# Optimization experiments

Hardware: AMD Instinct MI355X
Metric: run time of the kernel (lower is better)

## Reference

```python
import jax, jax.numpy as jnp
import numpy as np

N_BINS = 10
P = 2


def setup_inputs() -> dict:
    key = jax.random.key(0)
    k1, k2 = jax.random.split(key)
    N, C = 1_000_000, 80
    probas = jax.random.uniform(k1, (N, C), dtype=jnp.float32)
    labels = jax.random.randint(k2, (N,), 0, C, dtype=jnp.int64 if jax.config.jax_enable_x64 else jnp.int32)
    return {"probas": probas, "labels": labels}


def reference(probas, labels):
    n, c = probas.shape
    bins = jnp.linspace(0.0, 1.0, N_BINS + 1)
    # torch loop uses half-open-at-left bins: bin_start < p <= bin_end.
    # searchsorted(side='left') finds first bin edge >= p; subtract 1 -> bin index.
    # p == 0 maps to -1 (belongs to no bin), matching the torch masks.
    bin_idx = jnp.searchsorted(bins, probas, side="left") - 1  # [N, C]
    # route out-of-range (p==0) samples to a per-class trash slot N_BINS
    slots = N_BINS + 1
    seg = jnp.where(bin_idx >= 0, bin_idx, N_BINS) + jnp.arange(c)[None, :] * slots  # [N, C]
    flat_seg = seg.reshape(-1)
    num_seg = c * slots

    ones = jnp.ones((n * c,), dtype=jnp.float32)
    counts = jax.ops.segment_sum(ones, flat_seg, num_segments=num_seg).reshape(c, slots)[:, :N_BINS]
    sum_p = jax.ops.segment_sum(probas.reshape(-1), flat_seg, num_segments=num_seg).reshape(c, slots)[:, :N_BINS]
    correct = (labels[:, None] == jnp.arange(c)[None, :]).astype(jnp.float32)  # [N, C]
    sum_acc = jax.ops.segment_sum(correct.reshape(-1), flat_seg, num_segments=num_seg).reshape(c, slots)[:, :N_BINS]

    nonempty = counts > 0  # [C, N_BINS]
    denom = jnp.maximum(counts, 1.0)
    confs = sum_p / denom   # mean confidence per (class, bin); NaN slots masked below
    accs = sum_acc / denom  # accuracy per (class, bin)

    # calibration_error with bin_weight='samples': probas_bin = n_samples / nansum(n_samples)
    probas_bin = counts / jnp.sum(counts, axis=1, keepdims=True)
    # sq_ce per class = nansum(probas_bin * (conf - acc)**P)  (empty bins contribute 0)
    sq_ce = jnp.sum(jnp.where(nonempty, probas_bin * (confs - accs) ** P, 0.0), axis=1)  # [C]
    mce = jnp.mean(sq_ce) ** (1.0 / P)
    return mce
```

## Files before the change

kernel.cpp:

```cpp
#include <hip/hip_runtime.h>

#define NBINS  10
#define NCLS   80
#define NSLOTS (NCLS * NBINS)
#define QS     262144.0f

__global__ void __launch_bounds__(256)
mce_accum(const float4* __restrict__ probas,
          const int*    __restrict__ labels,
          unsigned long long* __restrict__ g_pack,
          unsigned int nvec) {
    __shared__ unsigned long long s_pack[NSLOTS];
    for (int i = threadIdx.x; i < NSLOTS; i += 256) s_pack[i] = 0ull;
    __syncthreads();

    const unsigned int S  = gridDim.x * 512u;
    unsigned int v0 = (blockIdx.x * 256u + threadIdx.x) * 2u;

#define PROC(VV, ROW, A, B, LAB)                                          \
    {                                                                     \
        int cbase  = (int)((VV) - (ROW) * 20u) * 4;                       \
        int labrel = (LAB) - cbase;                                       \
        int sbase  = cbase * NBINS;                                       \
        float pe[8] = {A.x, A.y, A.z, A.w, B.x, B.y, B.z, B.w};           \
        _Pragma("unroll")                                                 \
        for (int j = 0; j < 8; ++j) {                                     \
            float p = pe[j];                                              \
            int b = (int)(p * 10.0f);                                     \
            b = min(b, 9);                                                \
            unsigned int q = (unsigned int)__builtin_fmaf(p, QS, 0.5f);   \
            unsigned long long inc = (unsigned long long)q               \
                | (1ull << 40)                                            \
                | ((j == labrel) ? (1ull << 52) : 0ull);                  \
            atomicAdd(&s_pack[sbase + j * NBINS + b], inc);               \
        }                                                                 \
    }

    while (v0 + S < nvec) {
        unsigned int v1 = v0 + S;
        float4 a0 = probas[v0], b0 = probas[v0 + 1];
        float4 a1 = probas[v1], b1 = probas[v1 + 1];
        unsigned int r0 = v0 / 20u, r1 = v1 / 20u;
        int lab0 = labels[r0];
        int lab1 = labels[r1];
        PROC(v0, r0, a0, b0, lab0)
        PROC(v1, r1, a1, b1, lab1)
        v0 += 2u * S;
    }
    while (v0 < nvec) {
        float4 a0 = probas[v0], b0 = probas[v0 + 1];
        unsigned int r0 = v0 / 20u;
        int lab0 = labels[r0];
        PROC(v0, r0, a0, b0, lab0)
        v0 += S;
    }
#undef PROC

    __syncthreads();
    for (int i = threadIdx.x; i < NSLOTS; i += 256) {
        unsigned long long w = s_pack[i];
        if (w) {
            unsigned long long q   = w & 0xFFFFFFFFFFull;
            unsigned long long cnt = (w >> 40) & 0xFFFull;
            unsigned long long acc = w >> 52;
            atomicAdd(&g_pack[i], q | (cnt << 36) | (acc << 53));
        }
    }
}

__global__ void __launch_bounds__(128)
mce_finalize(const unsigned long long* __restrict__ g_pack,
             float* __restrict__ out) {
    __shared__ double s_ce[128];
    int c = threadIdx.x;
    double ce = 0.0;
    if (c < NCLS) {
        double total = 0.0;
        for (int b = 0; b < NBINS; ++b)
            total += (double)((g_pack[c * NBINS + b] >> 36) & 0x1FFFFull);
        for (int b = 0; b < NBINS; ++b) {
            unsigned long long w = g_pack[c * NBINS + b];
            unsigned int n = (unsigned int)((w >> 36) & 0x1FFFFull);
            if (n > 0u) {
                double fn   = (double)n;
                double conf = ((double)(w & 0xFFFFFFFFFull) * (1.0 / 262144.0)) / fn;
                double acc  = (double)(w >> 53) / fn;
                double d    = conf - acc;
                ce += (fn / total) * d * d;
            }
        }
    }
    s_ce[c] = ce;
    __syncthreads();
    for (int off = 64; off > 0; off >>= 1) {
        if (c < off) s_ce[c] += s_ce[c + off];
        __syncthreads();
    }
    if (c == 0) out[0] = (float)sqrt(s_ce[0] / (double)NCLS);
}

extern "C" void kernel_launch(void* const* d_in, const int* in_sizes, int n_in,
                              void* d_out, int out_size, void* d_ws, size_t ws_size,
                              hipStream_t stream) {
    const float4* probas = (const float4*)d_in[0];
    const int*    labels = (const int*)d_in[1];

    unsigned int nvec = (unsigned int)(in_sizes[0] / 4);

    unsigned long long* g_pack = (unsigned long long*)d_ws;
    hipMemsetAsync(d_ws, 0, NSLOTS * sizeof(unsigned long long), stream);

    mce_accum<<<1024, 256, 0, stream>>>(probas, labels, g_pack, nvec);
    mce_finalize<<<1, 128, 0, stream>>>(g_pack, (float*)d_out);
}
```

Measured before the change: 76.58 us.

## Restructure histogram accumulation with wave-window loads, double buffering, and separate label pass

Each wavefront now reads 256-float4 windows, with lanes striding by 64 so loads coalesce, and double-buffers the next window's loads behind the current atomics. The per-element label comparison is removed from the hot loop, and a separate per-block pass adds correctness counts by gathering the labeled probability for each row. Binning now truncates from a single scaled quantization (q>>16 with scale 655360), which drops the separate multiply and fma. The grid doubles to 2048 blocks. The window division assumes nvec is a multiple of 256 (1,000,000*80/4 is) and adds a scattered gather per row. The quantization change alters rounding and the overflow margin.

```diff
diff --git a/kernel.cpp b/kernel.cpp
--- a/kernel.cpp
+++ b/kernel.cpp
@@ -3,61 +3,89 @@
 #define NBINS  10
 #define NCLS   80
 #define NSLOTS (NCLS * NBINS)
-#define QS     262144.0f
+#define QSF    655360.0f
+#define NBLK   2048
+#define NTHR   256
 
-__global__ void __launch_bounds__(256)
+__global__ void __launch_bounds__(NTHR)
 mce_accum(const float4* __restrict__ probas,
           const int*    __restrict__ labels,
           unsigned long long* __restrict__ g_pack,
-          unsigned int nvec) {
+          unsigned int nwin,
+          unsigned int nrows,
+          unsigned int rows_per_blk) {
     __shared__ unsigned long long s_pack[NSLOTS];
-    for (int i = threadIdx.x; i < NSLOTS; i += 256) s_pack[i] = 0ull;
+    for (int i = threadIdx.x; i < NSLOTS; i += NTHR) s_pack[i] = 0ull;
     __syncthreads();
 
-    const unsigned int S  = gridDim.x * 512u;
-    unsigned int v0 = (blockIdx.x * 256u + threadIdx.x) * 2u;
+    const unsigned int lane   = threadIdx.x & 63u;
+    const unsigned int wid    = (blockIdx.x * NTHR + threadIdx.x) >> 6;
+    const unsigned int nwaves = gridDim.x * (NTHR / 64);
 
-#define PROC(VV, ROW, A, B, LAB)                                          \
-    {                                                                     \
-        int cbase  = (int)((VV) - (ROW) * 20u) * 4;                       \
-        int labrel = (LAB) - cbase;                                       \
-        int sbase  = cbase * NBINS;                                       \
-        float pe[8] = {A.x, A.y, A.z, A.w, B.x, B.y, B.z, B.w};           \
-        _Pragma("unroll")                                                 \
-        for (int j = 0; j < 8; ++j) {                                     \
-            float p = pe[j];                                              \
-            int b = (int)(p * 10.0f);                                     \
-            b = min(b, 9);                                                \
-            unsigned int q = (unsigned int)__builtin_fmaf(p, QS, 0.5f);   \
-            unsigned long long inc = (unsigned long long)q               \
-                | (1ull << 40)                                            \
-                | ((j == labrel) ? (1ull << 52) : 0ull);                  \
-            atomicAdd(&s_pack[sbase + j * NBINS + b], inc);               \
-        }                                                                 \
+#define LOADW(W, X0, X1, X2, X3, SB)                                   \
+    {                                                                  \
+        const float4* pw = probas + ((size_t)(W) * 256u + lane);       \
+        X0 = pw[0]; X1 = pw[64]; X2 = pw[128]; X3 = pw[192];           \
+        SB = (((W) * 256u + lane) % 20u) * 320u;                       \
     }
 
-    while (v0 + S < nvec) {
-        unsigned int v1 = v0 + S;
-        float4 a0 = probas[v0], b0 = probas[v0 + 1];
-        float4 a1 = probas[v1], b1 = probas[v1 + 1];
-        unsigned int r0 = v0 / 20u, r1 = v1 / 20u;
-        int lab0 = labels[r0];
-        int lab1 = labels[r1];
-        PROC(v0, r0, a0, b0, lab0)
-        PROC(v1, r1, a1, b1, lab1)
-        v0 += 2u * S;
+#define COMPUTE(X0, X1, X2, X3, SB)                                    \
+    {                                                                  \
+        float pe[16] = {X0.x, X0.y, X0.z, X0.w, X1.x, X1.y, X1.z, X1.w,\
+                        X2.x, X2.y, X2.z, X2.w, X3.x, X3.y, X3.z, X3.w};\
+        _Pragma("unroll")                                              \
+        for (int k = 0; k < 4; ++k) {                                  \
+            unsigned int sbk = (SB) + (unsigned int)k * 1280u;         \
+            sbk = min(sbk, sbk - 6400u);            \
+            _Pragma("unroll")                                          \
+            for (int j = 0; j < 4; ++j) {                              \
+                float p = pe[k * 4 + j];                               \
+                unsigned int q = (unsigned int)(p * QSF);              \
+                unsigned int t = min(q >> 16, 9u);                     \
+                unsigned long long inc = (unsigned long long)q | (1ull << 40); \
+                atomicAdd((unsigned long long*)((char*)s_pack + sbk    \
+                          + (t << 3) + 80 * j), inc);                  \
+            }                                                          \
+        }                                                              \
     }
-    while (v0 < nvec) {
-        float4 a0 = probas[v0], b0 = probas[v0 + 1];
-        unsigned int r0 = v0 / 20u;
-        int lab0 = labels[r0];
-        PROC(v0, r0, a0, b0, lab0)
-        v0 += S;
+
+    {
+        unsigned int w = wid;
+        float4 a0, a1, a2, a3, b0, b1, b2, b3;
+        unsigned int sbA, sbB;
+        LOADW(w, a0, a1, a2, a3, sbA)
+        for (;;) {
+            unsigned int wB = w + nwaves;
+            bool hB = wB < nwin;
+            if (hB) LOADW(wB, b0, b1, b2, b3, sbB)
+            COMPUTE(a0, a1, a2, a3, sbA)
+            if (!hB) break;
+            unsigned int wA = wB + nwaves;
+            bool hA = wA < nwin;
+            if (hA) LOADW(wA, a0, a1, a2, a3, sbA)
+            COMPUTE(b0, b1, b2, b3, sbB)
+            if (!hA) break;
+            w = wA;
+        }
     }
-#undef PROC
+#undef LOADW
+#undef COMPUTE
+
+    {
+        const float* pf = (const float*)probas;
+        unsigned int rend = min(blockIdx.x * rows_per_blk + rows_per_blk, nrows);
+        for (unsigned int r = blockIdx.x * rows_per_blk + threadIdx.x;
+             r < rend; r += NTHR) {
+            int lab = labels[r];
+            float p = pf[(size_t)r * NCLS + (unsigned int)lab];
+            unsigned int q = (unsigned int)(p * QSF);
+            unsigned int t = min(q >> 16, 9u);
+            atomicAdd(&s_pack[(unsigned int)lab * NBINS + t], 1ull << 52);
+        }
+    }
 
     __syncthreads();
-    for (int i = threadIdx.x; i < NSLOTS; i += 256) {
+    for (int i = threadIdx.x; i < NSLOTS; i += NTHR) {
         unsigned long long w = s_pack[i];
         if (w) {
             unsigned long long q   = w & 0xFFFFFFFFFFull;
@@ -83,7 +111,7 @@
             unsigned int n = (unsigned int)((w >> 36) & 0x1FFFFull);
             if (n > 0u) {
                 double fn   = (double)n;
-                double conf = ((double)(w & 0xFFFFFFFFFull) * (1.0 / 262144.0)) / fn;
+                double conf = ((double)(w & 0xFFFFFFFFFull) * (1.0 / 655360.0)) / fn;
                 double acc  = (double)(w >> 53) / fn;
                 double d    = conf - acc;
                 ce += (fn / total) * d * d;
@@ -105,11 +133,14 @@
     const float4* probas = (const float4*)d_in[0];
     const int*    labels = (const int*)d_in[1];
 
-    unsigned int nvec = (unsigned int)(in_sizes[0] / 4);
+    unsigned int nvec  = (unsigned int)(in_sizes[0] / 4);
+    unsigned int nwin  = nvec / 256u;
+    unsigned int nrows = (unsigned int)in_sizes[1];
+    unsigned int rpb   = (nrows + NBLK - 1) / NBLK;
 
     unsigned long long* g_pack = (unsigned long long*)d_ws;
     hipMemsetAsync(d_ws, 0, NSLOTS * sizeof(unsigned long long), stream);
 
-    mce_accum<<<1024, 256, 0, stream>>>(probas, labels, g_pack, nvec);
+    mce_accum<<<NBLK, NTHR, 0, stream>>>(probas, labels, g_pack, nwin, nrows, rpb);
     mce_finalize<<<1, 128, 0, stream>>>(g_pack, (float*)d_out);
 }
```

Result: slower. 88.50 us (+15.6%).

## Software-pipeline probas loads with double buffering and widen per-thread chunk

Applied to the files above, without the earlier changes.

Each thread now handles four float4 vectors (16 elements) per step and uses two register buffers. The next chunk's loads are issued before the current chunk's shared-memory atomics run, so global-memory latency overlaps with atomic work. The grid doubles to 2048 blocks. Register pressure goes up, which may lower occupancy, and doubling the block count doubles the number of global flush atomics.

```diff
diff --git a/kernel.cpp b/kernel.cpp
--- a/kernel.cpp
+++ b/kernel.cpp
@@ -4,65 +4,77 @@
 #define NCLS   80
 #define NSLOTS (NCLS * NBINS)
 #define QS     262144.0f
+#define NBLK   2048
+#define NTHR   256
 
-__global__ void __launch_bounds__(256)
+__global__ void __launch_bounds__(NTHR)
 mce_accum(const float4* __restrict__ probas,
           const int*    __restrict__ labels,
           unsigned long long* __restrict__ g_pack,
           unsigned int nvec) {
     __shared__ unsigned long long s_pack[NSLOTS];
-    for (int i = threadIdx.x; i < NSLOTS; i += 256) s_pack[i] = 0ull;
+    for (int i = threadIdx.x; i < NSLOTS; i += NTHR) s_pack[i] = 0ull;
     __syncthreads();
 
-    const unsigned int S  = gridDim.x * 512u;
-    unsigned int v0 = (blockIdx.x * 256u + threadIdx.x) * 2u;
+    const unsigned int S = gridDim.x * NTHR * 4u;
+    unsigned int w = (blockIdx.x * NTHR + threadIdx.x) * 4u;
 
-#define PROC(VV, ROW, A, B, LAB)                                          \
+#define LOADS(V, Q0, Q1, Q2, Q3, LAB)                                     \
     {                                                                     \
-        int cbase  = (int)((VV) - (ROW) * 20u) * 4;                       \
+        Q0 = probas[(V)];     Q1 = probas[(V) + 1];                       \
+        Q2 = probas[(V) + 2]; Q3 = probas[(V) + 3];                       \
+        LAB = labels[(V) / 20u];                                          \
+    }
+
+#define PROC(V, Q0, Q1, Q2, Q3, LAB)                                      \
+    {                                                                     \
+        unsigned int row = (V) / 20u;                                     \
+        int cbase  = (int)((V) - row * 20u) * 4;                          \
         int labrel = (LAB) - cbase;                                       \
         int sbase  = cbase * NBINS;                                       \
-        float pe[8] = {A.x, A.y, A.z, A.w, B.x, B.y, B.z, B.w};           \
+        float pe[16] = {Q0.x, Q0.y, Q0.z, Q0.w, Q1.x, Q1.y, Q1.z, Q1.w,   \
+                        Q2.x, Q2.y, Q2.z, Q2.w, Q3.x, Q3.y, Q3.z, Q3.w};  \
         _Pragma("unroll")                                                 \
-        for (int j = 0; j < 8; ++j) {                                     \
+        for (int j = 0; j < 16; ++j) {                                    \
             float p = pe[j];                                              \
             int b = (int)(p * 10.0f);                                     \
             b = min(b, 9);                                                \
             unsigned int q = (unsigned int)__builtin_fmaf(p, QS, 0.5f);   \
-            unsigned long long inc = (unsigned long long)q               \
+            unsigned long long inc = (unsigned long long)q                \
                 | (1ull << 40)                                            \
                 | ((j == labrel) ? (1ull << 52) : 0ull);                  \
             atomicAdd(&s_pack[sbase + j * NBINS + b], inc);               \
         }                                                                 \
     }
 
-    while (v0 + S < nvec) {
-        unsigned int v1 = v0 + S;
-        float4 a0 = probas[v0], b0 = probas[v0 + 1];
-        float4 a1 = probas[v1], b1 = probas[v1 + 1];
-        unsigned int r0 = v0 / 20u, r1 = v1 / 20u;
-        int lab0 = labels[r0];
-        int lab1 = labels[r1];
-        PROC(v0, r0, a0, b0, lab0)
-        PROC(v1, r1, a1, b1, lab1)
-        v0 += 2u * S;
+    {
+        float4 a0, a1, a2, a3, b0, b1, b2, b3;
+        int labA, labB;
+        LOADS(w, a0, a1, a2, a3, labA)
+        for (;;) {
+            unsigned int wB = w + S;
+            bool hB = wB < nvec;
+            if (hB) LOADS(wB, b0, b1, b2, b3, labB)
+            PROC(w, a0, a1, a2, a3, labA)
+            if (!hB) break;
+            unsigned int wA = wB + S;
+            bool hA = wA < nvec;
+            if (hA) LOADS(wA, a0, a1, a2, a3, labA)
+            PROC(wB, b0, b1, b2, b3, labB)
+            if (!hA) break;
+            w = wA;
+        }
     }
-    while (v0 < nvec) {
-        float4 a0 = probas[v0], b0 = probas[v0 + 1];
-        unsigned int r0 = v0 / 20u;
-        int lab0 = labels[r0];
-        PROC(v0, r0, a0, b0, lab0)
-        v0 += S;
-    }
+#undef LOADS
 #undef PROC
 
     __syncthreads();
-    for (int i = threadIdx.x; i < NSLOTS; i += 256) {
-        unsigned long long w = s_pack[i];
-        if (w) {
-            unsigned long long q   = w & 0xFFFFFFFFFFull;
-            unsigned long long cnt = (w >> 40) & 0xFFFull;
-            unsigned long long acc = w >> 52;
+    for (int i = threadIdx.x; i < NSLOTS; i += NTHR) {
+        unsigned long long v = s_pack[i];
+        if (v) {
+            unsigned long long q   = v & 0xFFFFFFFFFFull;
+            unsigned long long cnt = (v >> 40) & 0xFFFull;
+            unsigned long long acc = v >> 52;
             atomicAdd(&g_pack[i], q | (cnt << 36) | (acc << 53));
         }
     }
@@ -110,6 +122,6 @@
     unsigned long long* g_pack = (unsigned long long*)d_ws;
     hipMemsetAsync(d_ws, 0, NSLOTS * sizeof(unsigned long long), stream);
 
-    mce_accum<<<1024, 256, 0, stream>>>(probas, labels, g_pack, nvec);
+    mce_accum<<<NBLK, NTHR, 0, stream>>>(probas, labels, g_pack, nvec);
     mce_finalize<<<1, 128, 0, stream>>>(g_pack, (float*)d_out);
 }
```

Result: slower. 82.65 us (+7.9%).
